# Optimization experiments

Measured on AMD Instinct MI355X. Metric: run time of the kernel, lower is better.

The kernel has to match this reference:

```python
import jax, jax.numpy as jnp
import numpy as np

B, S, D, E, L = 4, 384, 300, 50, 2
HD = D // L  # head_dim = 150


def _linear_params(k, fin, fout):
    bnd = 1.0 / np.sqrt(fin)
    kw, kb = jax.random.split(k)
    W = jax.random.uniform(kw, (fout, fin), minval=-bnd, maxval=bnd, dtype=jnp.float32)
    b = jax.random.uniform(kb, (fout,), minval=-bnd, maxval=bnd, dtype=jnp.float32)
    return W, b


def setup_inputs() -> dict:
    key = jax.random.key(0)
    ks = jax.random.split(key, 6)
    W0, b0 = _linear_params(ks[0], D, HD)            # weight_list[0]: Linear(300, 150)
    W1, b1 = _linear_params(ks[1], D + HD, HD)       # weight_list[1]: Linear(450, 150)
    Wh, bh = _linear_params(ks[2], 2 * HD + E, E)    # Edgeupdate.W: Linear(350, 50)
    Wout, bout = _linear_params(ks[3], D, D)         # linear_output: Linear(300, 300)
    adj = jax.random.uniform(ks[4], (B, S, S, E), dtype=jnp.float32)
    gcn_inputs = jax.random.normal(ks[5], (B, S, D), dtype=jnp.float32)
    return dict(adj=adj, gcn_inputs=gcn_inputs, W0=W0, b0=b0, W1=W1, b1=b1,
                Wh=Wh, bh=bh, Wout=Wout, bout=bout)


def reference(adj, gcn_inputs, W0, b0, W1, b1, Wh, bh, Wout, bout):
    # Edgeupdate weight split: cat order is [edge(E), node1(HD), node2(HD)]
    Wh_e = Wh[:, :E]            # [E, E]
    Wh_1 = Wh[:, E:E + HD]      # [E, HD]
    Wh_2 = Wh[:, E + HD:]       # [E, HD]

    outputs = gcn_inputs        # [B, S, D]
    cache = [gcn_inputs]
    out_list = []
    for (Wl, bl) in ((W0, b0), (W1, b1)):
        e_dim = adj.shape[-1]
        # mean over edge channels of (adj_e @ outputs): einsum fuses the mean
        Ax = jnp.einsum('bike,bkd->bid', adj, outputs) / e_dim   # [B, S, din]
        # AxW = W_l(Ax) + W_l(outputs)  (same linear applied twice, bias twice)
        AxW = (Ax @ Wl.T + bl) + (outputs @ Wl.T + bl)           # [B, S, HD]
        gAxW = jax.nn.relu(AxW)
        # Edgeupdate highway: new_edge[b,i,j] = W([edge[b,i,j]; g[b,j]; g[b,i]]) + bh
        # (node1[b,i,j] = g[b,j], node2[b,i,j] = g[b,i] from the expand/permute)
        edge_part = adj @ Wh_e.T                                  # [B, S, S, E]
        n1 = gAxW @ Wh_1.T                                        # [B, S, E]
        n2 = gAxW @ Wh_2.T                                        # [B, S, E]
        adj = edge_part + n1[:, None, :, :] + n2[:, :, None, :] + bh
        cache.append(gAxW)
        outputs = jnp.concatenate(cache, axis=2)                  # growing concat
        out_list.append(gAxW)  # gcn_drop is identity in eval mode

    gcn_outputs = jnp.concatenate(out_list, axis=2) + gcn_inputs  # [B, S, D]
    return gcn_outputs @ Wout.T + bout
```

## Files before the change

kernel.cpp:

```cpp
#include <hip/hip_runtime.h>

constexpr int Bc  = 4;
constexpr int Sc  = 384;
constexpr int Dc  = 300;
constexpr int Ec  = 50;
constexpr int HDc = 150;
constexpr int WHC = 350;
constexpr int MT  = Bc * Sc;

typedef __attribute__((ext_vector_type(8))) short bf16x8;
typedef __attribute__((ext_vector_type(4))) float f32x4;

__device__ __forceinline__ short f2bf(float x) {
    union { float f; unsigned u; } v; v.f = x;
    unsigned r = (v.u + 0x7FFFu + ((v.u >> 16) & 1u)) >> 16;
    return (short)r;
}

__device__ __forceinline__ void s12_unit(const float* __restrict__ G,
                                         const float* __restrict__ sm,
                                         float* __restrict__ s12, int unit)
{
    int wave = threadIdx.x >> 6, lane = threadIdx.x & 63;
    int g = unit * 4 + wave;
    const float* gp = G + (long)g * Dc;
    float a = 0.f, c = 0.f;
    #pragma unroll
    for (int h0 = 0; h0 < HDc; h0 += 64) {
        int h = h0 + lane;
        if (h < HDc) { float v = gp[h]; a += v * sm[64 + h]; c += v * sm[224 + h]; }
    }
    #pragma unroll
    for (int off = 32; off; off >>= 1) {
        a += __shfl_down(a, off);
        c += __shfl_down(c, off);
    }
    if (lane == 0) { s12[2*g] = a; s12[2*g + 1] = c; }
}

template<int BSRC, int A1M, int HASD, int HASB, int RELU>
__device__ __forceinline__ void mgemm_body(
    short* As, short* Bs, int bx, int by, int b,
    const float* __restrict__ A, int lda, long sA,
    const float* __restrict__ Bw, int ldb, long sB,
    const float* __restrict__ W1a, const float* __restrict__ WoutP,
    const float* __restrict__ Dm, int ldd, long sD,
    const float* __restrict__ bias, float bscale,
    const float* __restrict__ s12, const float* __restrict__ sm,
    float* __restrict__ C, int ldc, long sC,
    int M, int N, int K)
{
    const float* Ap = A + (long)b * sA;
    const float* Bp = Bw + (long)b * sB;
    const float* Dp = Dm + (long)b * sD;
    float* Cp = C + (long)b * sC;

    const int tid  = threadIdx.x;
    const int wave = tid >> 6, lane = tid & 63;
    const int wm = wave & 1, wn = wave >> 1;
    const int lm = lane & 15, quad = lane >> 4;
    const int m0 = by * 32, n0 = bx * 32;

    const int srow = tid >> 3;
    const int sk   = (tid & 7) * 8;
    const int nc   = tid & 31;
    const int kr   = tid >> 5;

    float sbh = 0.f; const float* s1p = nullptr; float s2v = 0.f;
    if constexpr (A1M) {
        sbh = sm[384];
        s1p = s12 + 2L * Sc * b;
        s2v = s1p[2 * (m0 + srow) + 1];
    }

    float ra[8], rb[8];

    auto stageA = [&](int k0) {
        int am = m0 + srow;
        int kb = k0 + sk;
        if constexpr (A1M) {
            float4 u = *(const float4*)(Ap + (long)am * lda + kb);
            float4 w = *(const float4*)(Ap + (long)am * lda + kb + 4);
            const float* up = (const float*)&u;
            const float* wp = (const float*)&w;
            #pragma unroll
            for (int j = 0; j < 4; ++j) {
                ra[j]     = (up[j] + s1p[2*(kb + j)]     + s2v + sbh) * (1.0f/Ec);
                ra[4 + j] = (wp[j] + s1p[2*(kb + 4 + j)] + s2v + sbh) * (1.0f/Ec);
            }
        } else {
            if (kb + 7 < K) {
                float4 u = *(const float4*)(Ap + (long)am * lda + kb);
                float4 w = *(const float4*)(Ap + (long)am * lda + kb + 4);
                ra[0]=u.x; ra[1]=u.y; ra[2]=u.z; ra[3]=u.w;
                ra[4]=w.x; ra[5]=w.y; ra[6]=w.z; ra[7]=w.w;
            } else {
                #pragma unroll
                for (int j = 0; j < 8; ++j) {
                    int k = kb + j;
                    ra[j] = (k < K) ? Ap[(long)am * lda + k] : 0.f;
                }
            }
        }
    };

    auto stageB = [&](int k0) {
        if constexpr (BSRC == 0) {
            int n = n0 + nc;
            bool nok = n < N;
            #pragma unroll
            for (int p = 0; p < 8; ++p) {
                int k = k0 + kr + p * 8;
                rb[p] = nok ? Bp[(long)k * ldb + n] : 0.f;
            }
        } else {
            int nr = n0 + srow;
            bool nok = nr < N;
            const float* wp = Bp; int ld = ldb; int nn = nr;
            if constexpr (BSRC == 2) {
                if (nr < 150)      { wp = Bp;    ld = 300; nn = nr; }
                else if (nr < 300) { wp = W1a;   ld = 450; nn = nr - 150; }
                else               { wp = WoutP; ld = 300; nn = nr - 300; }
            }
            #pragma unroll
            for (int p = 0; p < 4; ++p) {
                int k = k0 + sk + 2 * p;
                if (nok && k + 1 < K) {
                    float2 v = *(const float2*)(wp + (long)nn * ld + k);
                    rb[2*p] = v.x; rb[2*p + 1] = v.y;
                } else {
                    rb[2*p]     = (nok && k < K)     ? wp[(long)nn * ld + k]     : 0.f;
                    rb[2*p + 1] = (nok && k + 1 < K) ? wp[(long)nn * ld + k + 1] : 0.f;
                }
            }
        }
    };

    auto stash = [&]() {
        #pragma unroll
        for (int j = 0; j < 8; ++j) As[srow * 72 + sk + j] = f2bf(ra[j]);
        if constexpr (BSRC == 0) {
            #pragma unroll
            for (int p = 0; p < 8; ++p) Bs[nc * 72 + kr + p * 8] = f2bf(rb[p]);
        } else {
            #pragma unroll
            for (int j = 0; j < 8; ++j) Bs[srow * 72 + sk + j] = f2bf(rb[j]);
        }
    };

    f32x4 acc = {0.f, 0.f, 0.f, 0.f};

    stageA(0); stageB(0);
    for (int k0 = 0; k0 < K; k0 += 64) {
        __syncthreads();
        stash();
        __syncthreads();
        if (k0 + 64 < K) { stageA(k0 + 64); stageB(k0 + 64); }
        {
            bf16x8 a0 = *(const bf16x8*)(As + (wm*16 + lm) * 72 + quad * 8);
            bf16x8 b0 = *(const bf16x8*)(Bs + (wn*16 + lm) * 72 + quad * 8);
            acc = __builtin_amdgcn_mfma_f32_16x16x32_bf16(a0, b0, acc, 0, 0, 0);
            bf16x8 a1 = *(const bf16x8*)(As + (wm*16 + lm) * 72 + 32 + quad * 8);
            bf16x8 b1 = *(const bf16x8*)(Bs + (wn*16 + lm) * 72 + 32 + quad * 8);
            acc = __builtin_amdgcn_mfma_f32_16x16x32_bf16(a1, b1, acc, 0, 0, 0);
        }
    }

    int cn = n0 + wn * 16 + lm;
    if (cn < N) {
        #pragma unroll
        for (int r = 0; r < 4; ++r) {
            int cm = m0 + wm * 16 + quad * 4 + r;
            if (cm < M) {
                float v = acc[r];
                if constexpr (HASD) v += Dp[(long)cm * ldd + cn];
                if constexpr (HASB) v += bscale * bias[cn];
                if constexpr (RELU) v = fmaxf(v, 0.f);
                Cp[(long)cm * ldc + cn] = v;
            }
        }
    }
}

template<int BSRC, int A1M, int HASD, int HASB, int RELU>
__global__ __launch_bounds__(256)
void mgemm(const float* __restrict__ A, int lda, long sA,
           const float* __restrict__ Bw, int ldb, long sB,
           const float* __restrict__ W1a, const float* __restrict__ WoutP,
           const float* __restrict__ Dm, int ldd, long sD,
           const float* __restrict__ bias, float bscale,
           const float* __restrict__ s12, const float* __restrict__ sm,
           float* __restrict__ C, int ldc, long sC,
           int M, int N, int K)
{
    __shared__ short As[32 * 72];
    __shared__ short Bs[32 * 72];
    mgemm_body<BSRC,A1M,HASD,HASB,RELU>(As, Bs,
        blockIdx.x, blockIdx.y, blockIdx.z,
        A, lda, sA, Bw, ldb, sB, W1a, WoutP, Dm, ldd, sD,
        bias, bscale, s12, sm, C, ldc, sC, M, N, K);
}

__global__ __launch_bounds__(256)
void fused1(const float* __restrict__ adj, const float* __restrict__ X,
            const float* __restrict__ W0, const float* __restrict__ W1,
            const float* __restrict__ Wout, const float* __restrict__ Wh,
            const float* __restrict__ bh,
            float* __restrict__ sm, float* __restrict__ A0,
            float* __restrict__ wadj, float* __restrict__ R)
{
    __shared__ float lds[64 * 51 + 64];
    const int bx = blockIdx.x, t = threadIdx.x;

    if (bx < 912) {
        short* As = (short*)lds;
        short* Bs = As + 32 * 72;
        mgemm_body<2,0,0,0,0>(As, Bs, bx % 19, bx / 19, 0,
            X, Dc, 0, W0, 300, 0, W1, Wout,
            nullptr, 0, 0, nullptr, 0.f, nullptr, nullptr,
            R, 600, 0, MT, 600, Dc);
    } else if (bx == 912) {
        for (int u = t; u < 512; u += 256) {
            if (u < Ec) {
                float s = 0.f;
                for (int e = 0; e < Ec; ++e) s += Wh[e*WHC + u];
                sm[u] = s;
            } else if (u >= 64 && u < 64 + HDc) {
                int h = u - 64; float s = 0.f;
                for (int e = 0; e < Ec; ++e) s += Wh[e*WHC + Ec + h];
                sm[u] = s;
            } else if (u >= 224 && u < 224 + HDc) {
                int h = u - 224; float s = 0.f;
                for (int e = 0; e < Ec; ++e) s += Wh[e*WHC + Ec + HDc + h];
                sm[u] = s;
            } else if (u == 384) {
                float s = 0.f;
                for (int e = 0; e < Ec; ++e) s += bh[e];
                sm[u] = s;
            }
        }
    } else {
        const int unit = bx - 913;
        float* tile = lds;
        float* wec  = lds + 64 * 51;

        long base = (long)unit * 3200;
        const float4* p4 = (const float4*)(adj + base);
        float4 v0 = p4[t];
        float4 v1 = p4[t + 256];
        float4 v2 = p4[t + 512];
        float4 v3 = {0.f, 0.f, 0.f, 0.f};
        if (t < 32) v3 = p4[t + 768];

        if (t < Ec) {
            float s = 0.f;
            for (int e = 0; e < Ec; ++e) s += Wh[e * WHC + t];
            wec[t] = s;
        }

        auto scat = [&](int i, const float4& v) {
            const float* vp = (const float*)&v;
            #pragma unroll
            for (int j = 0; j < 4; ++j) {
                int e = 4 * i + j;
                tile[(e / 50) * 51 + (e % 50)] = vp[j];
            }
        };
        scat(t, v0);
        scat(t + 256, v1);
        scat(t + 512, v2);
        if (t < 32) scat(t + 768, v3);
        __syncthreads();

        int r = t >> 2, q = t & 3;
        int h0 = q * 13, h1 = (q == 3) ? 50 : h0 + 13;
        const float* row = tile + r * 51;
        float s = 0.f, w = 0.f;
        for (int i = h0; i < h1; ++i) { float v = row[i]; s += v; w += v * wec[i]; }
        s += __shfl_xor(s, 1); w += __shfl_xor(w, 1);
        s += __shfl_xor(s, 2); w += __shfl_xor(w, 2);
        if (q == 0) {
            int g = unit * 64 + r;
            A0[g]   = s * (1.0f / Ec);
            wadj[g] = w;
        }
    }
}

__global__ __launch_bounds__(256)
void fused3(const float* __restrict__ Gbuf, const float* __restrict__ sm,
            float* __restrict__ s12, const float* __restrict__ W1,
            float* __restrict__ R, const float* __restrict__ Wout,
            const float* __restrict__ bout, float* __restrict__ out)
{
    __shared__ short As[32 * 72];
    __shared__ short Bs[32 * 72];
    const int bx = blockIdx.x;

    if (bx < 480) {
        mgemm_body<1,0,1,1,0>(As, Bs, bx % 10, bx / 10, 0,
            Gbuf, Dc, 0, Wout, Dc, 0, nullptr, nullptr,
            R + 2 * HDc, 600, 0, bout, 1.0f, nullptr, nullptr,
            out, Dc, 0, MT, Dc, HDc);
    } else if (bx < 480 + 240) {
        int v = bx - 480;
        mgemm_body<1,0,1,0,0>(As, Bs, v % 5, v / 5, 0,
            Gbuf, Dc, 0, W1 + Dc, Dc + HDc, 0, nullptr, nullptr,
            R + HDc, 600, 0, nullptr, 0.f, nullptr, nullptr,
            R + HDc, 600, 0, MT, HDc, HDc);
    } else {
        s12_unit(Gbuf, sm, s12, bx - 720);
    }
}

extern "C" void kernel_launch(void* const* d_in, const int* in_sizes, int n_in,
                              void* d_out, int out_size, void* d_ws, size_t ws_size,
                              hipStream_t stream) {
    const float* adj  = (const float*)d_in[0];
    const float* X    = (const float*)d_in[1];
    const float* W0   = (const float*)d_in[2];
    const float* b0   = (const float*)d_in[3];
    const float* W1   = (const float*)d_in[4];
    const float* b1   = (const float*)d_in[5];
    const float* Wh   = (const float*)d_in[6];
    const float* bh   = (const float*)d_in[7];
    const float* Wout = (const float*)d_in[8];
    const float* bout = (const float*)d_in[9];
    float* out = (float*)d_out;

    float* ws   = (float*)d_ws;
    float* sm   = ws;
    float* A0   = sm + 512;
    float* wadj = A0 + Bc * Sc * Sc;
    float* R    = wadj + Bc * Sc * Sc;
    float* Gbuf = R + (long)Bc * Sc * 600;
    float* s12  = Gbuf + (long)Bc * Sc * Dc;

    const long AS = (long)Sc * Sc;
    const long RS = (long)Sc * 600;
    const long GS = (long)Sc * Dc;

    fused1<<<912 + 1 + (Bc*Sc*Sc)/64, 256, 0, stream>>>(
        adj, X, W0, W1, Wout, Wh, bh, sm, A0, wadj, R);

    mgemm<0,0,1,1,1><<<dim3(5, 12, Bc), 256, 0, stream>>>(
        A0, Sc, AS, R, 600, RS, nullptr, nullptr,
        R, 600, RS, b0, 2.0f, nullptr, nullptr,
        Gbuf, Dc, GS, Sc, HDc, Sc);

    fused3<<<480 + 240 + 384, 256, 0, stream>>>(
        Gbuf, sm, s12, W1, R, Wout, bout, out);

    mgemm<0,1,1,1,1><<<dim3(5, 12, Bc), 256, 0, stream>>>(
        wadj, Sc, AS, R + HDc, 600, RS, nullptr, nullptr,
        R + HDc, 600, RS, b1, 2.0f, s12, sm,
        Gbuf + HDc, Dc, GS, Sc, HDc, Sc);

    mgemm<1,0,1,0,0><<<dim3(10, 48, 1), 256, 0, stream>>>(
        Gbuf + HDc, Dc, 0, Wout + HDc, Dc, 0, nullptr, nullptr,
        out, Dc, 0, nullptr, 0.f, nullptr, nullptr,
        out, Dc, 0, MT, Dc, HDc);
}
```

Baseline: 227.2 us.

## Double-buffer global prefetch registers and pack bf16 conversion in GEMM tile

```diff
diff --git a/kernel.cpp b/kernel.cpp
--- a/kernel.cpp
+++ b/kernel.cpp
@@ -15,6 +15,12 @@
     union { float f; unsigned u; } v; v.f = x;
     unsigned r = (v.u + 0x7FFFu + ((v.u >> 16) & 1u)) >> 16;
     return (short)r;
+}
+
+__device__ __forceinline__ unsigned cvtpk_bf16(float lo, float hi) {
+    unsigned r;
+    asm("v_cvt_pk_bf16_f32 %0, %1, %2" : "=v"(r) : "v"(lo), "v"(hi));
+    return r;
 }
 
 __device__ __forceinline__ void s12_unit(const float* __restrict__ G,
@@ -73,9 +79,21 @@
         s2v = s1p[2 * (m0 + srow) + 1];
     }
 
-    float ra[8], rb[8];
-
-    auto stageA = [&](int k0) {
+    const int cn = n0 + wn * 16 + lm;
+    float bpre = 0.f;
+    float dpre[4] = {0.f, 0.f, 0.f, 0.f};
+    if constexpr (HASB) { if (cn < N) bpre = bias[cn]; }
+    if constexpr (HASD) {
+        #pragma unroll
+        for (int r = 0; r < 4; ++r) {
+            int cm = m0 + wm * 16 + quad * 4 + r;
+            if (cn < N && cm < M) dpre[r] = Dp[(long)cm * ldd + cn];
+        }
+    }
+
+    float ra0[8], rb0[8], ra1[8], rb1[8];
+
+    auto stageA = [&](float* ra, int k0) {
         int am = m0 + srow;
         int kb = k0 + sk;
         if constexpr (A1M) {
@@ -104,7 +122,7 @@
         }
     };
 
-    auto stageB = [&](int k0) {
+    auto stageB = [&](float* rb, int k0) {
         if constexpr (BSRC == 0) {
             int n = n0 + nc;
             bool nok = n < N;
@@ -136,45 +154,57 @@
         }
     };
 
-    auto stash = [&]() {
+    auto stash = [&](float* ra, float* rb) {
         #pragma unroll
-        for (int j = 0; j < 8; ++j) As[srow * 72 + sk + j] = f2bf(ra[j]);
+        for (int j = 0; j < 8; j += 2)
+            *(unsigned*)(As + srow * 72 + sk + j) = cvtpk_bf16(ra[j], ra[j+1]);
         if constexpr (BSRC == 0) {
             #pragma unroll
             for (int p = 0; p < 8; ++p) Bs[nc * 72 + kr + p * 8] = f2bf(rb[p]);
         } else {
             #pragma unroll
-            for (int j = 0; j < 8; ++j) Bs[srow * 72 + sk + j] = f2bf(rb[j]);
+            for (int j = 0; j < 8; j += 2)
+                *(unsigned*)(Bs + srow * 72 + sk + j) = cvtpk_bf16(rb[j], rb[j+1]);
         }
     };
 
     f32x4 acc = {0.f, 0.f, 0.f, 0.f};
 
-    stageA(0); stageB(0);
-    for (int k0 = 0; k0 < K; k0 += 64) {
+    auto mfma_step = [&]() {
+        bf16x8 a0 = *(const bf16x8*)(As + (wm*16 + lm) * 72 + quad * 8);
+        bf16x8 b0 = *(const bf16x8*)(Bs + (wn*16 + lm) * 72 + quad * 8);
+        acc = __builtin_amdgcn_mfma_f32_16x16x32_bf16(a0, b0, acc, 0, 0, 0);
+        bf16x8 a1 = *(const bf16x8*)(As + (wm*16 + lm) * 72 + 32 + quad * 8);
+        bf16x8 b1 = *(const bf16x8*)(Bs + (wn*16 + lm) * 72 + 32 + quad * 8);
+        acc = __builtin_amdgcn_mfma_f32_16x16x32_bf16(a1, b1, acc, 0, 0, 0);
+    };
+
+    stageA(ra0, 0); stageB(rb0, 0);
+    if (64 < K) { stageA(ra1, 64); stageB(rb1, 64); }
+
+    for (int k0 = 0; k0 < K; k0 += 128) {
         __syncthreads();
-        stash();
+        stash(ra0, rb0);
         __syncthreads();
-        if (k0 + 64 < K) { stageA(k0 + 64); stageB(k0 + 64); }
-        {
-            bf16x8 a0 = *(const bf16x8*)(As + (wm*16 + lm) * 72 + quad * 8);
-            bf16x8 b0 = *(const bf16x8*)(Bs + (wn*16 + lm) * 72 + quad * 8);
-            acc = __builtin_amdgcn_mfma_f32_16x16x32_bf16(a0, b0, acc, 0, 0, 0);
-            bf16x8 a1 = *(const bf16x8*)(As + (wm*16 + lm) * 72 + 32 + quad * 8);
-            bf16x8 b1 = *(const bf16x8*)(Bs + (wn*16 + lm) * 72 + 32 + quad * 8);
-            acc = __builtin_amdgcn_mfma_f32_16x16x32_bf16(a1, b1, acc, 0, 0, 0);
-        }
-    }
-
-    int cn = n0 + wn * 16 + lm;
+        if (k0 + 128 < K) { stageA(ra0, k0 + 128); stageB(rb0, k0 + 128); }
+        mfma_step();
+        if (k0 + 64 < K) {
+            __syncthreads();
+            stash(ra1, rb1);
+            __syncthreads();
+            if (k0 + 192 < K) { stageA(ra1, k0 + 192); stageB(rb1, k0 + 192); }
+            mfma_step();
+        }
+    }
+
     if (cn < N) {
         #pragma unroll
         for (int r = 0; r < 4; ++r) {
             int cm = m0 + wm * 16 + quad * 4 + r;
             if (cm < M) {
                 float v = acc[r];
-                if constexpr (HASD) v += Dp[(long)cm * ldd + cn];
-                if constexpr (HASB) v += bscale * bias[cn];
+                if constexpr (HASD) v += dpre[r];
+                if constexpr (HASB) v += bscale * bpre;
                 if constexpr (RELU) v = fmaxf(v, 0.f);
                 Cp[(long)cm * ldc + cn] = v;
             }
```

Result: slower. 235.5 us (+3.7%).
